# Kernel optimization log

Measured on AMD Instinct MI355X. Metric: run time of the kernel, lower is better.

Reference implementation:

```python
import math
import jax, jax.numpy as jnp
import numpy as np
from jax import lax

# ---- static config (mirrors RPN init + typical torchvision anchor setup) ----
IMG_H = IMG_W = 800
LEVELS = [(200, 200, 4, 32), (100, 100, 8, 64), (50, 50, 16, 128), (25, 25, 32, 256), (13, 13, 64, 512)]  # (h, w, stride, anchor_size)
RATIOS = (0.5, 1.0, 2.0)
COUNTS = tuple(h * w * len(RATIOS) for (h, w, _, _) in LEVELS)  # (120000,30000,7500,1875,507)
A_TOTAL = sum(COUNTS)  # 159882
PRE_NMS = 2000
POST_NMS = 1000
NMS_THRESH = 0.7
MIN_SIZE = 1e-3
BBOX_CLIP = math.log(1000.0 / 16)


def make_anchors():
    parts = []
    for (h, w, stride, size) in LEVELS:
        ws = np.array([size * np.sqrt(1.0 / r) for r in RATIOS], np.float32)  # [3]
        hs = np.array([size * np.sqrt(r) for r in RATIOS], np.float32)
        sx = (np.arange(w, dtype=np.float32) + 0.5) * stride
        sy = (np.arange(h, dtype=np.float32) + 0.5) * stride
        cy, cx = np.meshgrid(sy, sx, indexing='ij')
        cx = cx.reshape(-1, 1)
        cy = cy.reshape(-1, 1)
        a = np.stack([cx - ws / 2, cy - hs / 2, cx + ws / 2, cy + hs / 2], axis=-1)  # [HW,3,4]
        parts.append(a.reshape(-1, 4))
    return np.concatenate(parts, 0).astype(np.float32)


def setup_inputs() -> dict:
    key = jax.random.key(0)
    k1, k2 = jax.random.split(key)
    scores = jax.random.normal(k1, (1, A_TOTAL), dtype=jnp.float32)
    deltas = jax.random.normal(k2, (A_TOTAL, 4), dtype=jnp.float32) * 0.5
    anchors = jnp.asarray(make_anchors())
    return {'scores': scores, 'deltas': deltas, 'anchors': anchors}


def _pairwise_iou(b):
    area = (b[:, 2] - b[:, 0]) * (b[:, 3] - b[:, 1])  # [K]
    lt = jnp.maximum(b[:, None, :2], b[None, :, :2])   # [K,K,2]
    rb = jnp.minimum(b[:, None, 2:], b[None, :, 2:])
    wh = jnp.maximum(rb - lt, 0.0)
    inter = wh[..., 0] * wh[..., 1]
    return inter / (area[:, None] + area[None, :] - inter)


def reference(scores, deltas, anchors):
    s_all = lax.stop_gradient(scores[0])  # original does cls.detach()
    # ---- box decode (torchvision-style) ----
    w = anchors[:, 2] - anchors[:, 0]
    h = anchors[:, 3] - anchors[:, 1]
    cx = anchors[:, 0] + 0.5 * w
    cy = anchors[:, 1] + 0.5 * h
    dx, dy = deltas[:, 0], deltas[:, 1]
    dw = jnp.minimum(deltas[:, 2], BBOX_CLIP)
    dh = jnp.minimum(deltas[:, 3], BBOX_CLIP)
    px = cx + dx * w
    py = cy + dy * h
    pw = jnp.exp(dw) * w
    ph = jnp.exp(dh) * h
    boxes = jnp.stack([px - 0.5 * pw, py - 0.5 * ph, px + 0.5 * pw, py + 0.5 * ph], axis=1)  # [A,4]
    # ---- per-level top-k over objectness ----
    idx_parts = []
    off = 0
    for c in COUNTS:
        k = min(PRE_NMS, c)
        _, ti = lax.top_k(lax.dynamic_slice_in_dim(s_all, off, c), k)
        idx_parts.append(ti + off)
        off += c
    top_idx = jnp.concatenate(idx_parts)  # [K=8382]
    K = top_idx.shape[0]
    s = s_all[top_idx]
    b = boxes[top_idx]
    # ---- clip to image + min-size validity (masked instead of compacted) ----
    b = jnp.stack([jnp.clip(b[:, 0], 0.0, IMG_W), jnp.clip(b[:, 1], 0.0, IMG_H),
                   jnp.clip(b[:, 2], 0.0, IMG_W), jnp.clip(b[:, 3], 0.0, IMG_H)], axis=1)
    valid = ((b[:, 2] - b[:, 0]) >= MIN_SIZE) & ((b[:, 3] - b[:, 1]) >= MIN_SIZE)
    # ---- per-level NMS offset; replicates original feature_mask[keep] indexing
    # (positional indexing into the full anchor-order level-id vector) ----
    fmask_full = np.concatenate([np.full(c, i, np.float32) for i, c in enumerate(COUNTS)])
    fmask = jnp.asarray(fmask_full[:K])
    box_max = jnp.max(jnp.where(valid[:, None], b, -jnp.inf))
    bn = b + (fmask * (box_max + 1.0))[:, None]
    # ---- greedy NMS on score-sorted candidates ----
    s_m = jnp.where(valid, s, -jnp.inf)
    order = jnp.argsort(-s_m)
    s_srt = s_m[order]
    b_srt = b[order]
    iou = _pairwise_iou(bn[order])  # [K,K] ~281MB
    ar = jnp.arange(K)

    def body(i, keep):
        sup = (iou[i] > NMS_THRESH) & (ar > i)
        return jnp.where(keep[i], keep & ~sup, keep)

    keep = lax.fori_loop(0, K, body, s_srt > -jnp.inf)
    final = jnp.where(keep, s_srt, -jnp.inf)
    out_s, oidx = lax.top_k(final, POST_NMS)  # top post_nms kept, score order; -inf pads
    out_b = b_srt[oidx]
    return out_b, out_s
```

## Files before the change

kernel.cpp:

```cpp
#include <hip/hip_runtime.h>
#include <math.h>

typedef unsigned int u32;
typedef unsigned long long u64;
typedef unsigned char u8;

#define K_TOT 8382
#define NCH 131
#define CAP 1024
#define EC 64
#define DC 8
#define GCAP 32768
#define IMGSZ 800.0f

__device__ __constant__ int LOFF[5] = {0, 120000, 150000, 157500, 159375};
__device__ __constant__ int LCNT[5] = {120000, 30000, 7500, 1875, 507};
__device__ __constant__ int KSEL[5] = {2000, 2000, 2000, 1875, 507};
__device__ __constant__ int SELB[5] = {0, 2000, 4000, 6000, 7875};
__device__ __constant__ int HBS[4] = {0, 118, 148, 156};
__device__ __constant__ int GBS[6] = {0, 118, 148, 156, 158, 159};

static __device__ __forceinline__ u32 fkey(float x) {
    u32 u = __float_as_uint(x);
    u32 m = (u32)(((int)u) >> 31) | 0x80000000u;
    return u ^ m;
}

static __device__ __forceinline__ int lvl_of(int s) {
    return (s < 2000) ? 0 : (s < 4000) ? 1 : (s < 6000) ? 2 : (s < 7875) ? 3 : 4;
}

static __device__ __forceinline__ u64 rdlane64(u64 v, int j) {
    u32 lo = (u32)__builtin_amdgcn_readlane((int)(u32)v, j);
    u32 hi = (u32)__builtin_amdgcn_readlane((int)(u32)(v >> 32), j);
    return ((u64)hi << 32) | (u64)lo;
}

static __device__ __forceinline__ void thresh_scan(const u32* hist, u32* scanbuf, int m,
                                                   u32 need, u32* sv, int t) {
    for (int i = t; i < m; i += 1024) scanbuf[i] = hist[m - 1 - i];
    __syncthreads();
    for (int ofs = 1; ofs < m; ofs <<= 1) {
        int i0 = t, i1 = t + 1024;
        u32 a0 = 0, a1 = 0;
        if (i0 < m && i0 >= ofs) a0 = scanbuf[i0 - ofs];
        if (i1 < m && i1 >= ofs) a1 = scanbuf[i1 - ofs];
        __syncthreads();
        if (i0 < m && i0 >= ofs) scanbuf[i0] += a0;
        if (i1 < m && i1 >= ofs) scanbuf[i1] += a1;
        __syncthreads();
    }
    for (int i = t; i < m; i += 1024) {
        u32 inc = scanbuf[i];
        u32 exc = i ? scanbuf[i - 1] : 0;
        if (inc >= need && exc < need) { sv[0] = (u32)(m - 1 - i); sv[1] = need - exc; }
    }
    __syncthreads();
}

__global__ __launch_bounds__(1024) void k_hist(const float* __restrict__ scores,
                                               u32* __restrict__ hist3) {
    __shared__ u32 lh[2048];
    int t = threadIdx.x;
    lh[t] = 0; lh[t + 1024] = 0;
    __syncthreads();
    int b = blockIdx.x;
    int l = (b < HBS[1]) ? 0 : (b < HBS[2]) ? 1 : 2;
    int i = (b - HBS[l]) * 1024 + t;
    if (i < LCNT[l]) atomicAdd(&lh[fkey(scores[LOFF[l] + i]) >> 21], 1u);
    __syncthreads();
    u32* h = hist3 + l * 2048;
    if (lh[t]) atomicAdd(&h[t], lh[t]);
    if (lh[t + 1024]) atomicAdd(&h[t + 1024], lh[t + 1024]);
}

__global__ __launch_bounds__(1024) void k_thresh(const u32* __restrict__ hist3,
                                                 u32* __restrict__ tinfo) {
    __shared__ u32 scanbuf[2048];
    __shared__ u32 sv[2];
    int l = blockIdx.x;
    int t = threadIdx.x;
    thresh_scan(hist3 + l * 2048, scanbuf, 2048, (u32)KSEL[l], sv, t);
    if (t == 0) { tinfo[l * 2] = sv[0]; tinfo[l * 2 + 1] = sv[1]; }
}

__global__ __launch_bounds__(1024) void k_gather(const float* __restrict__ scores,
                                                 const u32* __restrict__ tinfo,
                                                 u32* __restrict__ sel, u32* __restrict__ cgt,
                                                 u32* __restrict__ gcnt, u32* __restrict__ gidx,
                                                 u32* __restrict__ gkey) {
    int b = blockIdx.x;
    int l = (b < GBS[1]) ? 0 : (b < GBS[2]) ? 1 : (b < GBS[3]) ? 2 : (b < GBS[4]) ? 3 : 4;
    int i = (b - GBS[l]) * 1024 + threadIdx.x;
    if (i >= LCNT[l]) return;
    int off = LOFF[l], sb = SELB[l];
    if (l >= 3) { sel[sb + i] = (u32)(off + i); return; }
    u32 ky = fkey(scores[off + i]);
    u32 b1 = tinfo[l * 2];
    u32 top = ky >> 21;
    if (top > b1) {
        u32 p = atomicAdd(&cgt[l], 1u);
        sel[sb + p] = (u32)(off + i);
    } else if (top == b1) {
        u32 e = atomicAdd(&gcnt[l], 1u);
        if (e < GCAP) { gidx[l * GCAP + e] = (u32)i; gkey[l * GCAP + e] = ky; }
    }
}

__global__ __launch_bounds__(1024) void k_final(const u32* __restrict__ gidx,
                                                const u32* __restrict__ gkey,
                                                const u32* __restrict__ gcnt,
                                                const u32* __restrict__ tinfo,
                                                u32* __restrict__ sel) {
    __shared__ u32 hist[2048];
    __shared__ u32 scanbuf[2048];
    __shared__ u32 eqbuf[1024];
    __shared__ u32 sv[2];
    __shared__ u32 c2, ceq;
    int l = blockIdx.x;
    int t = threadIdx.x;
    int k = KSEL[l], sb = SELB[l], off = LOFF[l];
    u32 m = gcnt[l]; if (m > GCAP) m = GCAP;
    u32 b1 = tinfo[l * 2];
    u32 need = tinfo[l * 2 + 1];
    const u32* kb = gkey + l * GCAP;
    const u32* ib = gidx + l * GCAP;
    hist[t] = 0; hist[t + 1024] = 0; __syncthreads();
    for (u32 e = t; e < m; e += 1024) atomicAdd(&hist[(kb[e] >> 10) & 2047u], 1u);
    __syncthreads();
    thresh_scan(hist, scanbuf, 2048, need, sv, t);
    u32 b2 = sv[0], need2 = sv[1];
    __syncthreads();
    hist[t] = 0; __syncthreads();
    for (u32 e = t; e < m; e += 1024) {
        u32 ky = kb[e];
        if (((ky >> 10) & 2047u) == b2) atomicAdd(&hist[ky & 1023u], 1u);
    }
    __syncthreads();
    thresh_scan(hist, scanbuf, 1024, need2, sv, t);
    u32 T = (b1 << 21) | (b2 << 10) | sv[0];
    u32 take = sv[1];
    if (t == 0) { c2 = 0; ceq = 0; }
    __syncthreads();
    u32 nGTbin = need - take;
    u32 base2 = (u32)sb + (u32)k - need;
    for (u32 e = t; e < m; e += 1024) {
        u32 ky = kb[e];
        if (ky > T) { u32 p = atomicAdd(&c2, 1u); sel[base2 + p] = (u32)off + ib[e]; }
        else if (ky == T) { u32 q = atomicAdd(&ceq, 1u); if (q < 1024) eqbuf[q] = ib[e]; }
    }
    __syncthreads();
    if (t == 0) {
        int n = (ceq > 1024u) ? 1024 : (int)ceq;
        for (int a = 1; a < n; ++a) {
            u32 v = eqbuf[a]; int bq = a - 1;
            while (bq >= 0 && eqbuf[bq] > v) { eqbuf[bq + 1] = eqbuf[bq]; --bq; }
            eqbuf[bq + 1] = v;
        }
        for (u32 q = 0; q < take; ++q) sel[base2 + nGTbin + q] = (u32)off + eqbuf[q];
    }
}

__global__ void k_decode(const float* __restrict__ scores, const float4* __restrict__ deltas,
                         const float4* __restrict__ anchors, const u32* __restrict__ sel,
                         float4* __restrict__ candB, float* __restrict__ candS,
                         u32* __restrict__ candV, u32* __restrict__ candA) {
    int s = blockIdx.x * 256 + threadIdx.x;
    if (s >= K_TOT) return;
    u32 a = sel[s];
    float4 an = anchors[a];
    float4 dl = deltas[a];
    float sc = scores[a];
    float w = __fsub_rn(an.z, an.x), h = __fsub_rn(an.w, an.y);
    float cx = __fadd_rn(an.x, __fmul_rn(0.5f, w));
    float cy = __fadd_rn(an.y, __fmul_rn(0.5f, h));
    const float CLIPV = (float)4.1351665567423563;
    float dw = fminf(dl.z, CLIPV);
    float dh = fminf(dl.w, CLIPV);
    float px = __fadd_rn(cx, __fmul_rn(dl.x, w));
    float py = __fadd_rn(cy, __fmul_rn(dl.y, h));
    float pw = __fmul_rn((float)exp((double)dw), w);
    float ph = __fmul_rn((float)exp((double)dh), h);
    float x1 = __fsub_rn(px, __fmul_rn(0.5f, pw));
    float y1 = __fsub_rn(py, __fmul_rn(0.5f, ph));
    float x2 = __fadd_rn(px, __fmul_rn(0.5f, pw));
    float y2 = __fadd_rn(py, __fmul_rn(0.5f, ph));
    x1 = fminf(fmaxf(x1, 0.0f), IMGSZ);
    y1 = fminf(fmaxf(y1, 0.0f), IMGSZ);
    x2 = fminf(fmaxf(x2, 0.0f), IMGSZ);
    y2 = fminf(fmaxf(y2, 0.0f), IMGSZ);
    bool valid = (__fsub_rn(x2, x1) >= 0.001f) && (__fsub_rn(y2, y1) >= 0.001f);
    candB[s] = make_float4(x1, y1, x2, y2);
    candS[s] = sc;
    candV[s] = valid ? 1u : 0u;
    candA[s] = a;
}

__global__ __launch_bounds__(256) void k_rank_lvl(const float* __restrict__ candS,
                                                  const u32* __restrict__ candA,
                                                  u32* __restrict__ Praw) {
    __shared__ u64 tile[256];
    int l = blockIdx.z;
    int cnt = KSEL[l], base = SELB[l];
    int tx = blockIdx.x * 256;
    int ty = blockIdx.y * 256;
    if (tx >= cnt || ty >= cnt) return;
    int t = threadIdx.x;
    u64 Aj = ~0ull;
    if (tx + t < cnt) {
        int j = base + tx + t;
        Aj = ((u64)(~fkey(candS[j])) << 32) | (u64)candA[j];
    }
    tile[t] = Aj;
    __syncthreads();
    int si = ty + t;
    if (si >= cnt) return;
    int s = base + si;
    u64 A = ((u64)(~fkey(candS[s])) << 32) | (u64)candA[s];
    int r = 0;
#pragma unroll 8
    for (int q = 0; q < 256; ++q) r += (tile[q] < A);
    if (r) atomicAdd(&Praw[s], (u32)r);
}

__global__ __launch_bounds__(256) void k_rank_glob(const float* __restrict__ candS,
                                                   const u32* __restrict__ candV,
                                                   const u32* __restrict__ Praw,
                                                   u32* __restrict__ rank) {
    __shared__ u64 colB[256];
    int t = threadIdx.x;
    int cj = blockIdx.x * 256 + t;
    u64 B = ~0ull;
    if (cj < K_TOT) {
        u32 smk = candV[cj] ? fkey(candS[cj]) : 0x007FFFFFu;
        u32 Pj = (u32)SELB[lvl_of(cj)] + Praw[cj];
        B = ((u64)(~smk) << 32) | (u64)Pj;
    }
    colB[t] = B;
    __syncthreads();
    int s = blockIdx.y * 256 + t;
    if (s >= K_TOT) return;
    u32 smk = candV[s] ? fkey(candS[s]) : 0x007FFFFFu;
    u32 Ps = (u32)SELB[lvl_of(s)] + Praw[s];
    u64 myB = ((u64)(~smk) << 32) | (u64)Ps;
    int cnt = 0;
#pragma unroll 8
    for (int j = 0; j < 256; ++j) cnt += (colB[j] < myB);
    if (cnt) atomicAdd(&rank[s], (u32)cnt);
}

__global__ void k_scatter(const float4* __restrict__ candB, const float* __restrict__ candS,
                          const u32* __restrict__ candV, const u32* __restrict__ rank,
                          float4* __restrict__ sB, float* __restrict__ sArea,
                          float* __restrict__ sS, u32* __restrict__ sV) {
    int s = blockIdx.x * 256 + threadIdx.x;
    if (s >= K_TOT) return;
    u32 r = rank[s];
    float4 b = candB[s];
    float area = __fmul_rn(__fsub_rn(b.z, b.x), __fsub_rn(b.w, b.y));
    sB[r] = b; sArea[r] = area; sS[r] = candS[s]; sV[r] = candV[s];
}

__global__ void k_vwords(const u32* __restrict__ sV, u64* __restrict__ vwords) {
    int i = blockIdx.x * 64 + threadIdx.x;
    bool pred = (i < K_TOT) && sV[i];
    u64 bw = __ballot(pred);
    if (threadIdx.x == 0) vwords[blockIdx.x] = bw;
}

__global__ __launch_bounds__(256) void k_mask(const float4* __restrict__ sB,
                                              const float* __restrict__ sArea,
                                              u64* __restrict__ diag, u32* __restrict__ ecnt,
                                              ulonglong2* __restrict__ epack,
                                              u32* __restrict__ dcnt, u64* __restrict__ dmask,
                                              ulonglong2* __restrict__ dpack) {
    __shared__ float4 cb[64];
    __shared__ float ca[64];
    int wd = blockIdx.x;
    int t = threadIdx.x;
    if (t < 64) {
        int j = wd * 64 + t;
        if (j < K_TOT) { cb[t] = sB[j]; ca[t] = sArea[j]; }
        else { cb[t] = make_float4(0.f, 0.f, 0.f, 0.f); ca[t] = 0.f; }
    }
    __syncthreads();
    int i = blockIdx.y * 256 + t;
    if (i >= K_TOT) return;
    int dwr = i >> 6;
    if (wd < dwr) return;
    float4 bi = sB[i];
    float ai = sArea[i];
    u64 bits = 0;
    int jbase = wd * 64;
    for (int j2 = 0; j2 < 64; ++j2) {
        int j = jbase + j2;
        if (j > i && j < K_TOT) {
            float4 bj = cb[j2];
            float ltx = fmaxf(bi.x, bj.x), lty = fmaxf(bi.y, bj.y);
            float rbx = fminf(bi.z, bj.z), rby = fminf(bi.w, bj.w);
            float wx = fmaxf(__fsub_rn(rbx, ltx), 0.0f);
            float wy = fmaxf(__fsub_rn(rby, lty), 0.0f);
            float inter = __fmul_rn(wx, wy);
            if (inter > 0.0f) {
                float uni = __fsub_rn(__fadd_rn(ai, ca[j2]), inter);
                float iou = inter / uni;
                if (iou > 0.7f) bits |= (1ull << j2);
            }
        }
    }
    if (wd == dwr) {
        diag[i] = bits;
        if (bits != 0ull) {
            u32 p = atomicAdd(&dcnt[dwr], 1u);
            if (p < DC) dpack[dwr * DC + p] = make_ulonglong2((u64)(i & 63), bits);
            atomicOr(&dmask[dwr], 1ull << (i & 63));
        }
    } else if (bits != 0ull) {
        u32 p = atomicAdd(&ecnt[dwr], 1u);
        if (p < CAP) epack[dwr * CAP + p] = make_ulonglong2((u64)((i & 63) | (wd << 6)), bits);
    }
}

__global__ __launch_bounds__(64) void k_scan(const u64* __restrict__ diag,
                                             const u64* __restrict__ vwords,
                                             const u32* __restrict__ ecnt,
                                             const ulonglong2* __restrict__ epack,
                                             const u32* __restrict__ dcnt,
                                             const u64* __restrict__ dmask,
                                             const ulonglong2* __restrict__ dpack,
                                             u64* __restrict__ keepw) {
    __shared__ u64 sVw[NCH];
    __shared__ u32 sCnt[NCH];
    __shared__ u32 sDn[NCH];
    __shared__ u64 sDm[NCH];
    __shared__ ulonglong2 sEpack[NCH * EC];
    __shared__ ulonglong2 sDpack[NCH * DC];
    volatile __shared__ u64 sR[NCH];
    __shared__ u64 sKeep[NCH];
    int lane = threadIdx.x;
    {
        int i0 = lane, i1 = lane + 64, i2 = lane + 128;
        bool p2 = (i2 < NCH);
        u64 v0 = vwords[i0], v1 = vwords[i1], v2 = p2 ? vwords[i2] : 0;
        u32 c0 = ecnt[i0], c1 = ecnt[i1], c2 = p2 ? ecnt[i2] : 0;
        u32 d0 = dcnt[i0], d1 = dcnt[i1], d2 = p2 ? dcnt[i2] : 0;
        u64 m0 = dmask[i0], m1 = dmask[i1], m2 = p2 ? dmask[i2] : 0;
        sVw[i0] = v0; sCnt[i0] = (c0 > CAP) ? CAP : c0; sDn[i0] = d0; sDm[i0] = m0; sR[i0] = 0;
        sVw[i1] = v1; sCnt[i1] = (c1 > CAP) ? CAP : c1; sDn[i1] = d1; sDm[i1] = m1; sR[i1] = 0;
        if (p2) { sVw[i2] = v2; sCnt[i2] = (c2 > CAP) ? CAP : c2; sDn[i2] = d2; sDm[i2] = m2; sR[i2] = 0; }
    }
    for (int base = 0; base < NCH; base += 16) {
        ulonglong2 tmp[16];
        int nb = NCH - base; if (nb > 16) nb = 16;
#pragma unroll
        for (int b = 0; b < 16; ++b)
            if (b < nb) tmp[b] = epack[(size_t)(base + b) * CAP + lane];
#pragma unroll
        for (int b = 0; b < 16; ++b)
            if (b < nb) sEpack[(base + b) * EC + lane] = tmp[b];
    }
    for (int base = 0; base < NCH * DC; base += 64 * 8) {
        ulonglong2 tmp[8];
#pragma unroll
        for (int b = 0; b < 8; ++b) {
            int i = base + b * 64 + lane;
            if (i < NCH * DC) tmp[b] = dpack[i];
        }
#pragma unroll
        for (int b = 0; b < 8; ++b) {
            int i = base + b * 64 + lane;
            if (i < NCH * DC) sDpack[i] = tmp[b];
        }
    }
    __syncthreads();
    for (int c = 0; c < NCH; ++c) {
        u32 cnt = sCnt[c];
        u32 dn = sDn[c];
        ulonglong2 E = sEpack[c * EC + lane];
        ulonglong2 DP = (lane < DC) ? sDpack[c * DC + lane] : make_ulonglong2(~0ull, 0ull);
        u64 vw = sVw[c];
        u64 alive = vw & ~sR[c];
        if (dn) {
            if (dn <= (u32)DC) {
                u64 dm = sDm[c];
                u32 ml = ((u32)lane < dn) ? (u32)DP.x : 0xFFu;
                while (dm) {
                    int j = __builtin_ctzll(dm);
                    dm &= dm - 1;
                    if ((alive >> j) & 1ull) {
                        u64 selm = __ballot(ml == (u32)j);
                        int src = __builtin_ctzll(selm);
                        alive &= ~rdlane64(DP.y, src);
                    }
                }
            } else {
                int r = c * 64 + lane;
                u64 D = (r < K_TOT) ? diag[r] : 0ull;
                u64 nzd = __ballot(D != 0ull);
                while (nzd) {
                    int j = __builtin_ctzll(nzd);
                    nzd &= nzd - 1;
                    if ((alive >> j) & 1ull) alive &= ~rdlane64(D, j);
                }
            }
        }
        if (lane == 0) sKeep[c] = alive;
        if ((u32)lane < cnt && ((alive >> ((u32)E.x & 63u)) & 1ull))
            atomicOr((u64*)&sR[(u32)E.x >> 6], E.y);
        if (cnt > (u32)EC) {
            for (u32 e = (u32)EC + (u32)lane; e < cnt; e += 64u) {
                ulonglong2 Et = epack[(size_t)c * CAP + e];
                u32 pk = (u32)Et.x;
                if ((alive >> (pk & 63u)) & 1ull) atomicOr((u64*)&sR[pk >> 6], Et.y);
            }
        }
    }
    __syncthreads();
    for (int i = lane; i < NCH; i += 64) keepw[i] = sKeep[i];
}

__global__ __launch_bounds__(1024) void k_out(const u64* __restrict__ keepw,
                                              const float4* __restrict__ sB,
                                              const float* __restrict__ sS,
                                              float* __restrict__ out) {
    __shared__ u32 wpre[NCH + 1];
    int t = threadIdx.x;
    if (t == 0) {
        u32 run = 0;
        for (int w = 0; w < NCH; ++w) { wpre[w] = run; run += (u32)__popcll(keepw[w]); }
        wpre[NCH] = run;
    }
    __syncthreads();
    u32 nk = wpre[NCH];
    for (int i = t; i < K_TOT; i += 1024) {
        int w = i >> 6, b = i & 63;
        u64 kw = keepw[w];
        u32 kb = wpre[w] + (u32)__popcll(kw & ((1ull << b) - 1ull));
        bool kp = (kw >> b) & 1ull;
        if (kp) {
            if (kb < 1000u) {
                float4 bx = sB[i];
                out[kb * 4 + 0] = bx.x; out[kb * 4 + 1] = bx.y;
                out[kb * 4 + 2] = bx.z; out[kb * 4 + 3] = bx.w;
                out[4000 + kb] = sS[i];
            }
        } else {
            u32 q = (u32)i - kb;
            u32 slot = nk + q;
            if (slot < 1000u) {
                float4 bx = sB[i];
                out[slot * 4 + 0] = bx.x; out[slot * 4 + 1] = bx.y;
                out[slot * 4 + 2] = bx.z; out[slot * 4 + 3] = bx.w;
                out[4000 + slot] = -INFINITY;
            }
        }
    }
}

static constexpr size_t al256(size_t x) { return (x + 255) & ~(size_t)255; }
static constexpr size_t KB4 = (size_t)K_TOT * 4;
static constexpr size_t KB16 = (size_t)K_TOT * 16;
static constexpr size_t O_RANK = 0;
static constexpr size_t O_PRAW = al256(O_RANK + KB4);
static constexpr size_t O_ECNT = al256(O_PRAW + KB4);
static constexpr size_t O_DCNT = al256(O_ECNT + (size_t)NCH * 4);
static constexpr size_t O_DMASK = al256(O_DCNT + (size_t)NCH * 4);
static constexpr size_t O_HIST = al256(O_DMASK + (size_t)NCH * 8);
static constexpr size_t O_CGT = al256(O_HIST + (size_t)3 * 2048 * 4);
static constexpr size_t O_GCNT = al256(O_CGT + 3 * 4);
static constexpr size_t MEMSET_BYTES = al256(O_GCNT + 3 * 4);
static constexpr size_t O_TINFO = MEMSET_BYTES;
static constexpr size_t O_SEL = al256(O_TINFO + 6 * 4);
static constexpr size_t O_GIDX = al256(O_SEL + KB4);
static constexpr size_t O_GKEY = al256(O_GIDX + (size_t)3 * GCAP * 4);
static constexpr size_t O_CANDB = al256(O_GKEY + (size_t)3 * GCAP * 4);
static constexpr size_t O_CANDS = al256(O_CANDB + KB16);
static constexpr size_t O_CANDV = al256(O_CANDS + KB4);
static constexpr size_t O_CANDA = al256(O_CANDV + KB4);
static constexpr size_t O_SB = al256(O_CANDA + KB4);
static constexpr size_t O_SAREA = al256(O_SB + KB16);
static constexpr size_t O_SS = al256(O_SAREA + KB4);
static constexpr size_t O_SV = al256(O_SS + KB4);
static constexpr size_t O_VW = al256(O_SV + KB4);
static constexpr size_t O_KW = al256(O_VW + (size_t)NCH * 8);
static constexpr size_t O_DIAG = al256(O_KW + (size_t)NCH * 8);
static constexpr size_t O_EPACK = al256(O_DIAG + (size_t)(NCH * 64) * 8);
static constexpr size_t O_DPACK = al256(O_EPACK + (size_t)NCH * CAP * 16);

extern "C" void kernel_launch(void* const* d_in, const int* in_sizes, int n_in,
                              void* d_out, int out_size, void* d_ws, size_t ws_size,
                              hipStream_t stream) {
    const float* scores = (const float*)d_in[0];
    const float4* deltas = (const float4*)d_in[1];
    const float4* anchors = (const float4*)d_in[2];
    float* out = (float*)d_out;
    char* ws = (char*)d_ws;

    u32* rank = (u32*)(ws + O_RANK);
    u32* Praw = (u32*)(ws + O_PRAW);
    u32* ecnt = (u32*)(ws + O_ECNT);
    u32* dcnt = (u32*)(ws + O_DCNT);
    u64* dmask = (u64*)(ws + O_DMASK);
    u32* hist3 = (u32*)(ws + O_HIST);
    u32* cgt = (u32*)(ws + O_CGT);
    u32* gcnt = (u32*)(ws + O_GCNT);
    u32* tinfo = (u32*)(ws + O_TINFO);
    u32* sel = (u32*)(ws + O_SEL);
    u32* gidx = (u32*)(ws + O_GIDX);
    u32* gkey = (u32*)(ws + O_GKEY);
    float4* candB = (float4*)(ws + O_CANDB);
    float* candS = (float*)(ws + O_CANDS);
    u32* candV = (u32*)(ws + O_CANDV);
    u32* candA = (u32*)(ws + O_CANDA);
    float4* sB = (float4*)(ws + O_SB);
    float* sArea = (float*)(ws + O_SAREA);
    float* sS = (float*)(ws + O_SS);
    u32* sV = (u32*)(ws + O_SV);
    u64* vwords = (u64*)(ws + O_VW);
    u64* keepw = (u64*)(ws + O_KW);
    u64* diag = (u64*)(ws + O_DIAG);
    ulonglong2* epack = (ulonglong2*)(ws + O_EPACK);
    ulonglong2* dpack = (ulonglong2*)(ws + O_DPACK);

    hipMemsetAsync(ws, 0, MEMSET_BYTES, stream);

    const int NBLK = (K_TOT + 255) / 256;
    k_hist<<<156, 1024, 0, stream>>>(scores, hist3);
    k_thresh<<<3, 1024, 0, stream>>>(hist3, tinfo);
    k_gather<<<159, 1024, 0, stream>>>(scores, tinfo, sel, cgt, gcnt, gidx, gkey);
    k_final<<<3, 1024, 0, stream>>>(gidx, gkey, gcnt, tinfo, sel);
    k_decode<<<NBLK, 256, 0, stream>>>(scores, deltas, anchors, sel, candB, candS, candV, candA);
    k_rank_lvl<<<dim3(8, 8, 5), 256, 0, stream>>>(candS, candA, Praw);
    k_rank_glob<<<dim3(NBLK, NBLK), 256, 0, stream>>>(candS, candV, Praw, rank);
    k_scatter<<<NBLK, 256, 0, stream>>>(candB, candS, candV, rank, sB, sArea, sS, sV);
    k_vwords<<<NCH, 64, 0, stream>>>(sV, vwords);
    k_mask<<<dim3(NCH, NBLK), 256, 0, stream>>>(sB, sArea, diag, ecnt, epack, dcnt, dmask, dpack);
    k_scan<<<1, 64, 0, stream>>>(diag, vwords, ecnt, epack, dcnt, dmask, dpack, keepw);
    k_out<<<1, 1024, 0, stream>>>(keepw, sB, sS, out);
}
```

Measured before the change: 224.1 us.

## Fuse vwords into scatter, software-pipeline NMS scan loop, parallelize output prefix

Drops the k_vwords kernel by setting the valid bits with atomicOr directly in k_scatter; the vwords array moves into the memset region so it starts at zero. The serial single-wave k_scan loop now keeps per-chunk metadata in registers and reads it with readlane. It prefetches the next chunk's epack, dpack and removal word, and forwards same-chunk suppression bits through a ballot instead of waiting for the shared-memory atomics, which shortens the dependency chain on each iteration. k_out replaces its single-thread prefix over keep words with a parallel scan, at the cost of extra barriers and some added complexity in the scan loop.

```diff
diff --git a/kernel.cpp b/kernel.cpp
--- a/kernel.cpp
+++ b/kernel.cpp
@@ -30,6 +30,9 @@
     return (s < 2000) ? 0 : (s < 4000) ? 1 : (s < 6000) ? 2 : (s < 7875) ? 3 : 4;
 }
 
+static __device__ __forceinline__ u32 rdl32(u32 v, int j) {
+    return (u32)__builtin_amdgcn_readlane((int)v, j);
+}
 static __device__ __forceinline__ u64 rdlane64(u64 v, int j) {
     u32 lo = (u32)__builtin_amdgcn_readlane((int)(u32)v, j);
     u32 hi = (u32)__builtin_amdgcn_readlane((int)(u32)(v >> 32), j);
@@ -252,20 +255,14 @@
 __global__ void k_scatter(const float4* __restrict__ candB, const float* __restrict__ candS,
                           const u32* __restrict__ candV, const u32* __restrict__ rank,
                           float4* __restrict__ sB, float* __restrict__ sArea,
-                          float* __restrict__ sS, u32* __restrict__ sV) {
+                          float* __restrict__ sS, u64* __restrict__ vwords) {
     int s = blockIdx.x * 256 + threadIdx.x;
     if (s >= K_TOT) return;
     u32 r = rank[s];
     float4 b = candB[s];
     float area = __fmul_rn(__fsub_rn(b.z, b.x), __fsub_rn(b.w, b.y));
-    sB[r] = b; sArea[r] = area; sS[r] = candS[s]; sV[r] = candV[s];
-}
-
-__global__ void k_vwords(const u32* __restrict__ sV, u64* __restrict__ vwords) {
-    int i = blockIdx.x * 64 + threadIdx.x;
-    bool pred = (i < K_TOT) && sV[i];
-    u64 bw = __ballot(pred);
-    if (threadIdx.x == 0) vwords[blockIdx.x] = bw;
+    sB[r] = b; sArea[r] = area; sS[r] = candS[s];
+    if (candV[s]) atomicOr(&vwords[r >> 6], 1ull << (r & 63));
 }
 
 __global__ __launch_bounds__(256) void k_mask(const float4* __restrict__ sB,
@@ -329,25 +326,25 @@
                                              const u64* __restrict__ dmask,
                                              const ulonglong2* __restrict__ dpack,
                                              u64* __restrict__ keepw) {
-    __shared__ u64 sVw[NCH];
-    __shared__ u32 sCnt[NCH];
-    __shared__ u32 sDn[NCH];
-    __shared__ u64 sDm[NCH];
     __shared__ ulonglong2 sEpack[NCH * EC];
     __shared__ ulonglong2 sDpack[NCH * DC];
     volatile __shared__ u64 sR[NCH];
     __shared__ u64 sKeep[NCH];
     int lane = threadIdx.x;
+    u64 v0, v1, v2, m0, m1, m2;
+    u32 c0, c1, c2, d0, d1, d2;
     {
         int i0 = lane, i1 = lane + 64, i2 = lane + 128;
         bool p2 = (i2 < NCH);
-        u64 v0 = vwords[i0], v1 = vwords[i1], v2 = p2 ? vwords[i2] : 0;
-        u32 c0 = ecnt[i0], c1 = ecnt[i1], c2 = p2 ? ecnt[i2] : 0;
-        u32 d0 = dcnt[i0], d1 = dcnt[i1], d2 = p2 ? dcnt[i2] : 0;
-        u64 m0 = dmask[i0], m1 = dmask[i1], m2 = p2 ? dmask[i2] : 0;
-        sVw[i0] = v0; sCnt[i0] = (c0 > CAP) ? CAP : c0; sDn[i0] = d0; sDm[i0] = m0; sR[i0] = 0;
-        sVw[i1] = v1; sCnt[i1] = (c1 > CAP) ? CAP : c1; sDn[i1] = d1; sDm[i1] = m1; sR[i1] = 0;
-        if (p2) { sVw[i2] = v2; sCnt[i2] = (c2 > CAP) ? CAP : c2; sDn[i2] = d2; sDm[i2] = m2; sR[i2] = 0; }
+        v0 = vwords[i0]; v1 = vwords[i1]; v2 = p2 ? vwords[i2] : 0;
+        c0 = ecnt[i0]; c1 = ecnt[i1]; c2 = p2 ? ecnt[i2] : 0;
+        d0 = dcnt[i0]; d1 = dcnt[i1]; d2 = p2 ? dcnt[i2] : 0;
+        m0 = dmask[i0]; m1 = dmask[i1]; m2 = p2 ? dmask[i2] : 0;
+        if (c0 > CAP) c0 = CAP;
+        if (c1 > CAP) c1 = CAP;
+        if (c2 > CAP) c2 = CAP;
+        sR[i0] = 0; sR[i1] = 0;
+        if (p2) sR[i2] = 0;
     }
     for (int base = 0; base < NCH; base += 16) {
         ulonglong2 tmp[16];
@@ -373,16 +370,25 @@
         }
     }
     __syncthreads();
+    u64 r_cur = 0;
+    ulonglong2 E = sEpack[lane];
+    ulonglong2 DP = (lane < DC) ? sDpack[lane] : make_ulonglong2(~0ull, 0ull);
+    u32 cnt = rdl32(c0, 0), dn = rdl32(d0, 0);
+    u64 vw = rdlane64(v0, 0), dmw = rdlane64(m0, 0);
     for (int c = 0; c < NCH; ++c) {
-        u32 cnt = sCnt[c];
-        u32 dn = sDn[c];
-        ulonglong2 E = sEpack[c * EC + lane];
-        ulonglong2 DP = (lane < DC) ? sDpack[c * DC + lane] : make_ulonglong2(~0ull, 0ull);
-        u64 vw = sVw[c];
-        u64 alive = vw & ~sR[c];
+        int cn = (c + 1 < NCH) ? (c + 1) : c;
+        u64 rpre = sR[cn];
+        ulonglong2 En = sEpack[cn * EC + lane];
+        ulonglong2 DPn = (lane < DC) ? sDpack[cn * DC + lane] : make_ulonglong2(~0ull, 0ull);
+        u32 cntn, dnn; u64 vwn, dmn;
+        if (cn < 64)       { cntn = rdl32(c0, cn);       dnn = rdl32(d0, cn);       vwn = rdlane64(v0, cn);       dmn = rdlane64(m0, cn); }
+        else if (cn < 128) { cntn = rdl32(c1, cn - 64);  dnn = rdl32(d1, cn - 64);  vwn = rdlane64(v1, cn - 64);  dmn = rdlane64(m1, cn - 64); }
+        else               { cntn = rdl32(c2, cn - 128); dnn = rdl32(d2, cn - 128); vwn = rdlane64(v2, cn - 128); dmn = rdlane64(m2, cn - 128); }
+
+        u64 alive = vw & ~r_cur;
         if (dn) {
             if (dn <= (u32)DC) {
-                u64 dm = sDm[c];
+                u64 dm = dmw & alive;
                 u32 ml = ((u32)lane < dn) ? (u32)DP.x : 0xFFu;
                 while (dm) {
                     int j = __builtin_ctzll(dm);
@@ -397,6 +403,7 @@
                 int r = c * 64 + lane;
                 u64 D = (r < K_TOT) ? diag[r] : 0ull;
                 u64 nzd = __ballot(D != 0ull);
+                nzd &= alive;
                 while (nzd) {
                     int j = __builtin_ctzll(nzd);
                     nzd &= nzd - 1;
@@ -405,15 +412,28 @@
             }
         }
         if (lane == 0) sKeep[c] = alive;
-        if ((u32)lane < cnt && ((alive >> ((u32)E.x & 63u)) & 1ull))
-            atomicOr((u64*)&sR[(u32)E.x >> 6], E.y);
+        u32 tc = (u32)E.x >> 6;
+        bool act = ((u32)lane < cnt) && (((alive >> ((u32)E.x & 63u)) & 1ull) != 0ull);
+        if (act) atomicOr((u64*)&sR[tc], E.y);
+        bool redo = false;
         if (cnt > (u32)EC) {
             for (u32 e = (u32)EC + (u32)lane; e < cnt; e += 64u) {
                 ulonglong2 Et = epack[(size_t)c * CAP + e];
                 u32 pk = (u32)Et.x;
                 if ((alive >> (pk & 63u)) & 1ull) atomicOr((u64*)&sR[pk >> 6], Et.y);
             }
-        }
+            redo = true;
+        }
+        u64 selm = __ballot(act && (tc == (u32)cn));
+        u64 contrib = 0;
+        while (selm) {
+            int j = __builtin_ctzll(selm);
+            selm &= selm - 1;
+            contrib |= rdlane64(E.y, j);
+        }
+        if (redo) rpre = sR[cn];
+        r_cur = rpre | contrib;
+        E = En; DP = DPn; cnt = cntn; dn = dnn; vw = vwn; dmw = dmn;
     }
     __syncthreads();
     for (int i = lane; i < NCH; i += 64) keepw[i] = sKeep[i];
@@ -423,19 +443,30 @@
                                               const float4* __restrict__ sB,
                                               const float* __restrict__ sS,
                                               float* __restrict__ out) {
-    __shared__ u32 wpre[NCH + 1];
-    int t = threadIdx.x;
-    if (t == 0) {
-        u32 run = 0;
-        for (int w = 0; w < NCH; ++w) { wpre[w] = run; run += (u32)__popcll(keepw[w]); }
-        wpre[NCH] = run;
-    }
-    __syncthreads();
-    u32 nk = wpre[NCH];
+    __shared__ u64 skw[NCH];
+    __shared__ u32 pc[NCH + 1];
+    int t = threadIdx.x;
+    if (t < NCH) {
+        u64 kw = keepw[t];
+        skw[t] = kw;
+        pc[t + 1] = (u32)__popcll(kw);
+    }
+    if (t == 0) pc[0] = 0;
+    __syncthreads();
+    for (int ofs = 1; ofs < NCH; ofs <<= 1) {
+        int i = t + 1;
+        u32 v = 0;
+        bool p = (t < NCH) && (i - ofs >= 1);
+        if (p) v = pc[i - ofs];
+        __syncthreads();
+        if (p) pc[i] += v;
+        __syncthreads();
+    }
+    u32 nk = pc[NCH];
     for (int i = t; i < K_TOT; i += 1024) {
         int w = i >> 6, b = i & 63;
-        u64 kw = keepw[w];
-        u32 kb = wpre[w] + (u32)__popcll(kw & ((1ull << b) - 1ull));
+        u64 kw = skw[w];
+        u32 kb = pc[w] + (u32)__popcll(kw & ((1ull << b) - 1ull));
         bool kp = (kw >> b) & 1ull;
         if (kp) {
             if (kb < 1000u) {
@@ -465,7 +496,8 @@
 static constexpr size_t O_ECNT = al256(O_PRAW + KB4);
 static constexpr size_t O_DCNT = al256(O_ECNT + (size_t)NCH * 4);
 static constexpr size_t O_DMASK = al256(O_DCNT + (size_t)NCH * 4);
-static constexpr size_t O_HIST = al256(O_DMASK + (size_t)NCH * 8);
+static constexpr size_t O_VW = al256(O_DMASK + (size_t)NCH * 8);
+static constexpr size_t O_HIST = al256(O_VW + (size_t)NCH * 8);
 static constexpr size_t O_CGT = al256(O_HIST + (size_t)3 * 2048 * 4);
 static constexpr size_t O_GCNT = al256(O_CGT + 3 * 4);
 static constexpr size_t MEMSET_BYTES = al256(O_GCNT + 3 * 4);
@@ -480,9 +512,7 @@
 static constexpr size_t O_SB = al256(O_CANDA + KB4);
 static constexpr size_t O_SAREA = al256(O_SB + KB16);
 static constexpr size_t O_SS = al256(O_SAREA + KB4);
-static constexpr size_t O_SV = al256(O_SS + KB4);
-static constexpr size_t O_VW = al256(O_SV + KB4);
-static constexpr size_t O_KW = al256(O_VW + (size_t)NCH * 8);
+static constexpr size_t O_KW = al256(O_SS + KB4);
 static constexpr size_t O_DIAG = al256(O_KW + (size_t)NCH * 8);
 static constexpr size_t O_EPACK = al256(O_DIAG + (size_t)(NCH * 64) * 8);
 static constexpr size_t O_DPACK = al256(O_EPACK + (size_t)NCH * CAP * 16);
@@ -501,6 +531,7 @@
     u32* ecnt = (u32*)(ws + O_ECNT);
     u32* dcnt = (u32*)(ws + O_DCNT);
     u64* dmask = (u64*)(ws + O_DMASK);
+    u64* vwords = (u64*)(ws + O_VW);
     u32* hist3 = (u32*)(ws + O_HIST);
     u32* cgt = (u32*)(ws + O_CGT);
     u32* gcnt = (u32*)(ws + O_GCNT);
@@ -515,8 +546,6 @@
     float4* sB = (float4*)(ws + O_SB);
     float* sArea = (float*)(ws + O_SAREA);
     float* sS = (float*)(ws + O_SS);
-    u32* sV = (u32*)(ws + O_SV);
-    u64* vwords = (u64*)(ws + O_VW);
     u64* keepw = (u64*)(ws + O_KW);
     u64* diag = (u64*)(ws + O_DIAG);
     ulonglong2* epack = (ulonglong2*)(ws + O_EPACK);
@@ -532,8 +561,7 @@
     k_decode<<<NBLK, 256, 0, stream>>>(scores, deltas, anchors, sel, candB, candS, candV, candA);
     k_rank_lvl<<<dim3(8, 8, 5), 256, 0, stream>>>(candS, candA, Praw);
     k_rank_glob<<<dim3(NBLK, NBLK), 256, 0, stream>>>(candS, candV, Praw, rank);
-    k_scatter<<<NBLK, 256, 0, stream>>>(candB, candS, candV, rank, sB, sArea, sS, sV);
-    k_vwords<<<NCH, 64, 0, stream>>>(sV, vwords);
+    k_scatter<<<NBLK, 256, 0, stream>>>(candB, candS, candV, rank, sB, sArea, sS, vwords);
     k_mask<<<dim3(NCH, NBLK), 256, 0, stream>>>(sB, sArea, diag, ecnt, epack, dcnt, dmask, dpack);
     k_scan<<<1, 64, 0, stream>>>(diag, vwords, ecnt, epack, dcnt, dmask, dpack, keepw);
     k_out<<<1, 1024, 0, stream>>>(keepw, sB, sS, out);
```

After: 228.1 us. No clear change (+1.8%).
